# Performance work log

Measured on AMD Instinct MI355X. Metric: run time of the kernel, lower is better.

Reference implementation:

```python
import jax, jax.numpy as jnp
import numpy as np

B, N, K = 4, 65536, 16
HIDDEN = 64


def setup_inputs() -> dict:
    key = jax.random.key(0)
    k1, k2, k3, k4 = jax.random.split(key, 4)
    pos = jax.random.normal(k1, (B, 3, N), dtype=jnp.float32)
    idx = jax.random.randint(k2, (B, N, K), 0, N, dtype=jnp.int64)
    dist = jax.random.uniform(k3, (B, N, K), dtype=jnp.float32)
    W = jax.random.normal(k4, (10, HIDDEN), dtype=jnp.float32) * (1.0 / np.sqrt(10.0))
    b = jnp.zeros((HIDDEN,), dtype=jnp.float32)
    return {"pos": pos, "idx": idx, "dist": dist, "W": W, "b": b}


def reference(pos, idx, dist, W, b):
    xyz = pos[:, :3, :]                                  # [B, 3, N]
    # gather neighbor coords: neighbors[b, c, n, k] = xyz[b, c, idx[b, n, k]]
    neighbors = jax.vmap(lambda x, i: x[:, i])(xyz, idx)  # [B, 3, N, K]
    ext_xyz = jnp.broadcast_to(xyz[:, :, :, None], neighbors.shape)
    concat = jnp.concatenate(
        [ext_xyz, neighbors, ext_xyz - neighbors, dist[:, None, :, :]], axis=1
    )                                                    # [B, 10, N, K]
    feat = jnp.max(concat, axis=-1)                      # [B, 10, N]
    feat = jnp.transpose(feat, (0, 2, 1))                # [B, N, 10]
    return jax.nn.relu(feat @ W + b)                     # [B, N, HIDDEN]
```

## Files before the change

### kernel.cpp

```cpp
#include <hip/hip_runtime.h>

#define NPTS 65536
#define NB_SHIFT 16
#define KNBR 16
#define HID 64

__global__ __launch_bounds__(256) void xyzt_kernel(const float* __restrict__ pos,
                                                   float4* __restrict__ xyzt) {
    int g = blockIdx.x * 256 + threadIdx.x;
    int b = g >> NB_SHIFT;
    int n = g & (NPTS - 1);
    const float* p = pos + (size_t)b * 3 * NPTS;
    float4 v;
    v.x = p[n];
    v.y = p[n + NPTS];
    v.z = p[n + 2 * NPTS];
    v.w = 0.f;
    xyzt[((size_t)b << NB_SHIFT) + n] = v;
}

template <int USE_T>
__global__ __launch_bounds__(256) void point_embed_kernel(
    const float*  __restrict__ pos,
    const float4* __restrict__ xyzt,
    const int*    __restrict__ idx,
    const float*  __restrict__ dist,
    const float*  __restrict__ W,
    const float*  __restrict__ bias,
    float*        __restrict__ out) {
    __shared__ float feat[256 * 12];
    const int tid = threadIdx.x;

    const int blk = ((int)blockIdx.x % 8) * 128 + ((int)blockIdx.x / 8);
    const int g = blk * 256 + tid;
    const int b = g >> NB_SHIFT;
    const int n = g & (NPTS - 1);

    const int hq = tid & 15;
    float4 Wv[10];
#pragma unroll
    for (int c = 0; c < 10; ++c)
        Wv[c] = ((const float4*)(W + c * HID))[hq];
    const float4 bv = ((const float4*)bias)[hq];

    const int4* iv = (const int4*)idx + (size_t)g * 4;
    int4 i0 = iv[0], i1 = iv[1], i2 = iv[2], i3 = iv[3];
    const float4* dv = (const float4*)dist + (size_t)g * 4;
    float4 d0 = dv[0], d1 = dv[1], d2 = dv[2], d3 = dv[3];
    float maxd = fmaxf(
        fmaxf(fmaxf(fmaxf(d0.x, d0.y), fmaxf(d0.z, d0.w)),
              fmaxf(fmaxf(d1.x, d1.y), fmaxf(d1.z, d1.w))),
        fmaxf(fmaxf(fmaxf(d2.x, d2.y), fmaxf(d2.z, d2.w)),
              fmaxf(fmaxf(d3.x, d3.y), fmaxf(d3.z, d3.w))));

    float cx, cy, cz;
    float mxx = -INFINITY, mxy = -INFINITY, mxz = -INFINITY;
    float mnx = INFINITY, mny = INFINITY, mnz = INFINITY;

    if (USE_T) {
        const float4* xb = xyzt + ((size_t)b << NB_SHIFT);
        float4 c = xb[n];
        cx = c.x; cy = c.y; cz = c.z;
#define GATH(J)                                   \
    {                                             \
        float4 q = xb[(J)];                       \
        mxx = fmaxf(mxx, q.x);                    \
        mxy = fmaxf(mxy, q.y);                    \
        mxz = fmaxf(mxz, q.z);                    \
        mnx = fminf(mnx, q.x);                    \
        mny = fminf(mny, q.y);                    \
        mnz = fminf(mnz, q.z);                    \
    }
        GATH(i0.x) GATH(i0.y) GATH(i0.z) GATH(i0.w)
        GATH(i1.x) GATH(i1.y) GATH(i1.z) GATH(i1.w)
        GATH(i2.x) GATH(i2.y) GATH(i2.z) GATH(i2.w)
        GATH(i3.x) GATH(i3.y) GATH(i3.z) GATH(i3.w)
#undef GATH
    } else {
        const float* px = pos + (size_t)b * 3 * NPTS;
        cx = px[n]; cy = px[n + NPTS]; cz = px[n + 2 * NPTS];
#define GATH(J)                                   \
    {                                             \
        float qx = px[(J)];                       \
        float qy = px[(J) + NPTS];                \
        float qz = px[(J) + 2 * NPTS];            \
        mxx = fmaxf(mxx, qx);                     \
        mxy = fmaxf(mxy, qy);                     \
        mxz = fmaxf(mxz, qz);                     \
        mnx = fminf(mnx, qx);                     \
        mny = fminf(mny, qy);                     \
        mnz = fminf(mnz, qz);                     \
    }
        GATH(i0.x) GATH(i0.y) GATH(i0.z) GATH(i0.w)
        GATH(i1.x) GATH(i1.y) GATH(i1.z) GATH(i1.w)
        GATH(i2.x) GATH(i2.y) GATH(i2.z) GATH(i2.w)
        GATH(i3.x) GATH(i3.y) GATH(i3.z) GATH(i3.w)
#undef GATH
    }

    float* f = feat + tid * 12;
    f[0] = cx;       f[1] = cy;       f[2] = cz;
    f[3] = mxx;      f[4] = mxy;      f[5] = mxz;
    f[6] = cx - mnx; f[7] = cy - mny; f[8] = cz - mnz;
    f[9] = maxd;     f[10] = 0.f;     f[11] = 0.f;
    __syncthreads();

    const int prow = tid >> 4;
    const size_t outbase = (size_t)blk * 256 * HID;
#pragma unroll
    for (int i = 0; i < 16; ++i) {
        const int p = i * 16 + prow;
        const float* fp = feat + p * 12;
        float4 acc = bv;
#pragma unroll
        for (int c = 0; c < 10; ++c) {
            const float fv = fp[c];
            acc.x += fv * Wv[c].x;
            acc.y += fv * Wv[c].y;
            acc.z += fv * Wv[c].z;
            acc.w += fv * Wv[c].w;
        }
        acc.x = fmaxf(acc.x, 0.f);
        acc.y = fmaxf(acc.y, 0.f);
        acc.z = fmaxf(acc.z, 0.f);
        acc.w = fmaxf(acc.w, 0.f);
        ((float4*)(out + outbase + (size_t)p * HID))[hq] = acc;
    }
}

extern "C" void kernel_launch(void* const* d_in, const int* in_sizes, int n_in,
                              void* d_out, int out_size, void* d_ws, size_t ws_size,
                              hipStream_t stream) {
    const float* pos  = (const float*)d_in[0];
    const int*   idx  = (const int*)d_in[1];
    const float* dist = (const float*)d_in[2];
    const float* W    = (const float*)d_in[3];
    const float* bias = (const float*)d_in[4];
    float* out = (float*)d_out;

    const int total   = in_sizes[0] / 3;
    const int nblocks = total / 256;
    const size_t need = (size_t)total * sizeof(float4);

    if (ws_size >= need) {
        xyzt_kernel<<<nblocks, 256, 0, stream>>>(pos, (float4*)d_ws);
        point_embed_kernel<1><<<nblocks, 256, 0, stream>>>(
            pos, (const float4*)d_ws, idx, dist, W, bias, out);
    } else {
        point_embed_kernel<0><<<nblocks, 256, 0, stream>>>(
            pos, nullptr, idx, dist, W, bias, out);
    }
}
```

Measured before the change: 121.9 us.

## Use nontemporal loads/stores, SoA shared features, and remapped block order in prep

Streaming loads of idx and dist and the output stores become nontemporal, so this single-use traffic is kept from displacing the xyzt table that the gathers hit. The shared feature buffer goes from per-point rows of 12 to a padded channel-major [10][257] layout, which changes the LDS bank access pattern on the write and read sides. The xyzt prep kernel now uses the same interleaved block ordering as the main kernel and nontemporal loads of pos. Nontemporal hints may not change anything if the hardware treats the streams the same way.

```diff
diff --git a/kernel.cpp b/kernel.cpp
--- a/kernel.cpp
+++ b/kernel.cpp
@@ -5,16 +5,21 @@
 #define KNBR 16
 #define HID 64
 
+typedef int   i32x4 __attribute__((ext_vector_type(4)));
+typedef float f32x4 __attribute__((ext_vector_type(4)));
+
 __global__ __launch_bounds__(256) void xyzt_kernel(const float* __restrict__ pos,
                                                    float4* __restrict__ xyzt) {
-    int g = blockIdx.x * 256 + threadIdx.x;
-    int b = g >> NB_SHIFT;
-    int n = g & (NPTS - 1);
+    const int tid = threadIdx.x;
+    const int blk = ((int)blockIdx.x & 7) * 128 + ((int)blockIdx.x >> 3);
+    const int g = blk * 256 + tid;
+    const int b = g >> NB_SHIFT;
+    const int n = g & (NPTS - 1);
     const float* p = pos + (size_t)b * 3 * NPTS;
     float4 v;
-    v.x = p[n];
-    v.y = p[n + NPTS];
-    v.z = p[n + 2 * NPTS];
+    v.x = __builtin_nontemporal_load(p + n);
+    v.y = __builtin_nontemporal_load(p + n + NPTS);
+    v.z = __builtin_nontemporal_load(p + n + 2 * NPTS);
     v.w = 0.f;
     xyzt[((size_t)b << NB_SHIFT) + n] = v;
 }
@@ -28,10 +33,10 @@
     const float*  __restrict__ W,
     const float*  __restrict__ bias,
     float*        __restrict__ out) {
-    __shared__ float feat[256 * 12];
+    __shared__ float feat[10][257];
     const int tid = threadIdx.x;
 
-    const int blk = ((int)blockIdx.x % 8) * 128 + ((int)blockIdx.x / 8);
+    const int blk = ((int)blockIdx.x & 7) * 128 + ((int)blockIdx.x >> 3);
     const int g = blk * 256 + tid;
     const int b = g >> NB_SHIFT;
     const int n = g & (NPTS - 1);
@@ -43,10 +48,16 @@
         Wv[c] = ((const float4*)(W + c * HID))[hq];
     const float4 bv = ((const float4*)bias)[hq];
 
-    const int4* iv = (const int4*)idx + (size_t)g * 4;
-    int4 i0 = iv[0], i1 = iv[1], i2 = iv[2], i3 = iv[3];
-    const float4* dv = (const float4*)dist + (size_t)g * 4;
-    float4 d0 = dv[0], d1 = dv[1], d2 = dv[2], d3 = dv[3];
+    const i32x4* iv = (const i32x4*)idx + (size_t)g * 4;
+    i32x4 i0 = __builtin_nontemporal_load(iv + 0);
+    i32x4 i1 = __builtin_nontemporal_load(iv + 1);
+    i32x4 i2 = __builtin_nontemporal_load(iv + 2);
+    i32x4 i3 = __builtin_nontemporal_load(iv + 3);
+    const f32x4* dv = (const f32x4*)dist + (size_t)g * 4;
+    f32x4 d0 = __builtin_nontemporal_load(dv + 0);
+    f32x4 d1 = __builtin_nontemporal_load(dv + 1);
+    f32x4 d2 = __builtin_nontemporal_load(dv + 2);
+    f32x4 d3 = __builtin_nontemporal_load(dv + 3);
     float maxd = fmaxf(
         fmaxf(fmaxf(fmaxf(d0.x, d0.y), fmaxf(d0.z, d0.w)),
               fmaxf(fmaxf(d1.x, d1.y), fmaxf(d1.z, d1.w))),
@@ -98,11 +109,16 @@
 #undef GATH
     }
 
-    float* f = feat + tid * 12;
-    f[0] = cx;       f[1] = cy;       f[2] = cz;
-    f[3] = mxx;      f[4] = mxy;      f[5] = mxz;
-    f[6] = cx - mnx; f[7] = cy - mny; f[8] = cz - mnz;
-    f[9] = maxd;     f[10] = 0.f;     f[11] = 0.f;
+    feat[0][tid] = cx;
+    feat[1][tid] = cy;
+    feat[2][tid] = cz;
+    feat[3][tid] = mxx;
+    feat[4][tid] = mxy;
+    feat[5][tid] = mxz;
+    feat[6][tid] = cx - mnx;
+    feat[7][tid] = cy - mny;
+    feat[8][tid] = cz - mnz;
+    feat[9][tid] = maxd;
     __syncthreads();
 
     const int prow = tid >> 4;
@@ -110,21 +126,22 @@
 #pragma unroll
     for (int i = 0; i < 16; ++i) {
         const int p = i * 16 + prow;
-        const float* fp = feat + p * 12;
         float4 acc = bv;
 #pragma unroll
         for (int c = 0; c < 10; ++c) {
-            const float fv = fp[c];
+            const float fv = feat[c][p];
             acc.x += fv * Wv[c].x;
             acc.y += fv * Wv[c].y;
             acc.z += fv * Wv[c].z;
             acc.w += fv * Wv[c].w;
         }
-        acc.x = fmaxf(acc.x, 0.f);
-        acc.y = fmaxf(acc.y, 0.f);
-        acc.z = fmaxf(acc.z, 0.f);
-        acc.w = fmaxf(acc.w, 0.f);
-        ((float4*)(out + outbase + (size_t)p * HID))[hq] = acc;
+        f32x4 av;
+        av.x = fmaxf(acc.x, 0.f);
+        av.y = fmaxf(acc.y, 0.f);
+        av.z = fmaxf(acc.z, 0.f);
+        av.w = fmaxf(acc.w, 0.f);
+        __builtin_nontemporal_store(av,
+            (f32x4*)(out + outbase + (size_t)p * HID) + hq);
     }
 }
 
```

Measured after the change: 128.8 us. 1.06x slower.
